# Kernel optimization log

Measured on AMD Instinct MI355X. Metric: run time of the kernel, lower is better.

The kernel has to match this reference:

```python
import jax, jax.numpy as jnp
import numpy as np

T = 100      # time steps
IC = 21      # input channels
NS = 7       # strikes
CF = 64      # cnn filters
H = 128      # lstm hidden
EPS = 1e-5


def conv1d(x, w, b):
    # x: (N, C, W), w: (O, I, 3), 'same' padding
    y = jax.lax.conv_general_dilated(x, w, window_strides=(1,), padding=[(1, 1)],
                                     dimension_numbers=('NCH', 'OIH', 'NCH'))
    return y + b[None, :, None]


def bn_eval(x, g, b, m, v):
    # eval-mode batchnorm over channel dim of (N, C, W)
    inv = g / jnp.sqrt(v + EPS)
    return x * inv[None, :, None] + (b - m * inv)[None, :, None]


def lstm_dir(xs, wih, whh, bih, bhh, reverse):
    # xs: (T, B, F); PyTorch gate order i, f, g, o
    B = xs.shape[1]
    h0 = jnp.zeros((B, H), xs.dtype)

    def step(carry, xt):
        h, c = carry
        gates = xt @ wih.T + h @ whh.T + (bih + bhh)
        i, f, g, o = jnp.split(gates, 4, axis=-1)
        c = jax.nn.sigmoid(f) * c + jax.nn.sigmoid(i) * jnp.tanh(g)
        h = jax.nn.sigmoid(o) * jnp.tanh(c)
        return (h, c), h

    _, hs = jax.lax.scan(step, (h0, h0), xs, reverse=reverse)
    return hs  # (T, B, H), aligned to input time order


def setup_inputs() -> dict:
    key = jax.random.key(0)
    ks = iter(jax.random.split(key, 64))

    def n(shape, s=0.05):
        return jax.random.normal(next(ks), shape, dtype=jnp.float32) * s

    d = {}
    d['x'] = jax.random.normal(next(ks), (512, T, IC, NS), dtype=jnp.float32)
    d['c1w'] = n((CF, IC, 3)); d['c1b'] = n((CF,))
    d['g1'] = 1.0 + n((CF,)); d['b1'] = n((CF,))
    d['m1'] = n((CF,)); d['v1'] = 1.0 + 0.1 * jax.random.uniform(next(ks), (CF,), dtype=jnp.float32)
    d['c2w'] = n((CF, CF, 3)); d['c2b'] = n((CF,))
    d['g2'] = 1.0 + n((CF,)); d['b2'] = n((CF,))
    d['m2'] = n((CF,)); d['v2'] = 1.0 + 0.1 * jax.random.uniform(next(ks), (CF,), dtype=jnp.float32)
    for layer, in_dim in ((0, CF * NS), (1, 2 * H)):
        for tag in ('f', 'b'):
            d[f'wih{layer}{tag}'] = n((4 * H, in_dim))
            d[f'whh{layer}{tag}'] = n((4 * H, H))
            d[f'bih{layer}{tag}'] = n((4 * H,))
            d[f'bhh{layer}{tag}'] = n((4 * H,))
    d['fc1w'] = n((64, 2 * H)); d['fc1b'] = n((64,))
    d['fc2w'] = n((2, 64)); d['fc2b'] = n((2,))
    return d


def reference(x, c1w, c1b, g1, b1, m1, v1, c2w, c2b, g2, b2, m2, v2,
              wih0f, whh0f, bih0f, bhh0f, wih0b, whh0b, bih0b, bhh0b,
              wih1f, whh1f, bih1f, bhh1f, wih1b, whh1b, bih1b, bhh1b,
              fc1w, fc1b, fc2w, fc2b):
    B = x.shape[0]
    # time-batched CNN: (B,T,IC,NS) -> (B*T, IC, NS); kernel (1,3) on H=1 slab == 1D conv
    h = x.reshape(B * T, IC, NS)
    h = jax.nn.relu(bn_eval(conv1d(h, c1w, c1b), g1, b1, m1, v1))
    h = jax.nn.relu(bn_eval(conv1d(h, c2w, c2b), g2, b2, m2, v2))
    # AdaptiveAvgPool2d((1, NS)) on (B,CF,1,NS) is identity; flatten -> (T,B,CF*NS)
    seq = h.reshape(B, T, CF * NS).transpose(1, 0, 2)
    # layer 0 bidirectional LSTM
    seq = jnp.concatenate([lstm_dir(seq, wih0f, whh0f, bih0f, bhh0f, False),
                           lstm_dir(seq, wih0b, whh0b, bih0b, bhh0b, True)], axis=-1)
    # layer 1 bidirectional LSTM (inter-layer dropout disabled: eval mode)
    seq = jnp.concatenate([lstm_dir(seq, wih1f, whh1f, bih1f, bhh1f, False),
                           lstm_dir(seq, wih1b, whh1b, bih1b, bhh1b, True)], axis=-1)
    last = seq[-1]                                    # (B, 2H)
    out = jax.nn.relu(last @ fc1w.T + fc1b)           # dropout = identity (eval)
    return out @ fc2w.T + fc2b                        # (B, 2)
```

## Files before the change

### kernel.cpp

```cpp
#include <hip/hip_runtime.h>

#define T_STEPS 100
#define IC      21
#define NS      7
#define CF      64
#define HID     128
#define EPS     1e-5f

#define OFF_W0FH   0
#define OFF_W0FL   114688
#define OFF_W0BH   229376
#define OFF_W0BL   344064
#define OFF_W1FH   458752
#define OFF_W1FL   524288
#define OFF_W1BH   589824
#define OFF_W1BL   655360
#define OFF_W1T    720896
#define OFF_W2T    724928
#define OFF_SCALE1 737216
#define OFF_SHIFT1 737280
#define OFF_SCALE2 737344
#define OFF_SHIFT2 737408
#define OFF_BIASL0 737472
#define OFF_BIAS1F 738496
#define OFF_BIAS1B 739008
#define PARAM_END  739520
#define OFF_H1F    739520
#define OFF_XP1B   805056
#define OFF_STATE  1067200
#define ZERO_TOTAL 393216
#define OFF_SEQ1BH 1460416
#define OFF_SEQ1BL 4737216
#define OFF_DYN    8014016

#define NB_PREP    1441792
#define NF_PREP    411840

typedef __attribute__((ext_vector_type(8))) short short8;
typedef __attribute__((ext_vector_type(4))) float f32x4;

__device__ __forceinline__ float sigmoidf_(float x) { return 1.0f / (1.0f + __expf(-x)); }
__device__ __forceinline__ float tanhf_(float x)    { return 2.0f / (1.0f + __expf(-2.0f * x)) - 1.0f; }

__device__ __forceinline__ unsigned short f2bf_rn(float f) {
    union { float f; unsigned int u; } v; v.f = f;
    unsigned int u = v.u;
    return (unsigned short)((u + 0x7FFFu + ((u >> 16) & 1u)) >> 16);
}
__device__ __forceinline__ float bf2f(unsigned short h) {
    union { unsigned int u; float f; } v; v.u = ((unsigned int)h) << 16;
    return v.f;
}

__device__ __forceinline__ void gload16(const void* g, void* l) {
    __builtin_amdgcn_global_load_lds(
        (const __attribute__((address_space(1))) unsigned int*)g,
        (__attribute__((address_space(3))) unsigned int*)l, 16, 0, 0);
}

__global__ void prep_kernel(
    const float* __restrict__ c1w, const float* __restrict__ c1b,
    const float* __restrict__ g1, const float* __restrict__ b1,
    const float* __restrict__ m1, const float* __restrict__ v1,
    const float* __restrict__ c2w, const float* __restrict__ c2b,
    const float* __restrict__ g2, const float* __restrict__ b2,
    const float* __restrict__ m2, const float* __restrict__ v2,
    const float* __restrict__ wih0f, const float* __restrict__ wih0b,
    const float* __restrict__ wih1f, const float* __restrict__ wih1b,
    const float* __restrict__ bih0f, const float* __restrict__ bhh0f,
    const float* __restrict__ bih0b, const float* __restrict__ bhh0b,
    const float* __restrict__ bih1f, const float* __restrict__ bhh1f,
    const float* __restrict__ bih1b, const float* __restrict__ bhh1b,
    float* __restrict__ ws)
{
    unsigned short* wsH = (unsigned short*)ws;
    int stride = gridDim.x * blockDim.x;
    for (int i = blockIdx.x * blockDim.x + threadIdx.x;
         i < NB_PREP + NF_PREP; i += stride) {
        if (i < NB_PREP) {
            float val; size_t dst; bool lo;
            if (i < 917504) {
                int plane = i / 229376;
                int ii = i - plane * 229376;
                int n = ii / 448, kk = ii - n * 448;
                int p = kk >> 6, oc = kk & 63;
                const float* src = (plane < 2) ? wih0f : wih0b;
                val = src[n * 448 + oc * 7 + p];
                int base = (plane == 0) ? OFF_W0FH : (plane == 1) ? OFF_W0FL
                         : (plane == 2) ? OFF_W0BH : OFF_W0BL;
                dst = (size_t)base * 2 + ii;
                lo = (plane & 1);
            } else {
                int e = i - 917504;
                int plane = e / 131072;
                int ii = e - plane * 131072;
                const float* src = (plane < 2) ? wih1f : wih1b;
                val = src[ii];
                int base = (plane == 0) ? OFF_W1FH : (plane == 1) ? OFF_W1FL
                         : (plane == 2) ? OFF_W1BH : OFF_W1BL;
                dst = (size_t)base * 2 + ii;
                lo = (plane & 1);
            }
            unsigned short hi = f2bf_rn(val);
            wsH[dst] = lo ? f2bf_rn(val - bf2f(hi)) : hi;
        } else {
            int j = i - NB_PREP;
            if (j < 4032) {
                int oc = j & 63, w = j >> 6;
                ws[OFF_W1T + j] = c1w[oc * 63 + w];
            } else if (j < 16320) {
                int jj = j - 4032;
                int oc = jj & 63, w = jj >> 6;
                ws[OFF_W2T + jj] = c2w[oc * 192 + w];
            } else if (j < 16384) {
                int oc = j - 16320;
                ws[OFF_SCALE1 + oc] = g1[oc] * rsqrtf(v1[oc] + EPS);
            } else if (j < 16448) {
                int oc = j - 16384;
                float inv = g1[oc] * rsqrtf(v1[oc] + EPS);
                ws[OFF_SHIFT1 + oc] = c1b[oc] * inv + b1[oc] - m1[oc] * inv;
            } else if (j < 16512) {
                int oc = j - 16448;
                ws[OFF_SCALE2 + oc] = g2[oc] * rsqrtf(v2[oc] + EPS);
            } else if (j < 16576) {
                int oc = j - 16512;
                float inv = g2[oc] * rsqrtf(v2[oc] + EPS);
                ws[OFF_SHIFT2 + oc] = c2b[oc] * inv + b2[oc] - m2[oc] * inv;
            } else if (j < 17600) {
                int n = j - 16576;
                ws[OFF_BIASL0 + n] = (n < 512) ? (bih0f[n] + bhh0f[n])
                                               : (bih0b[n - 512] + bhh0b[n - 512]);
            } else if (j < 18112) {
                int n = j - 17600;
                ws[OFF_BIAS1F + n] = bih1f[n] + bhh1f[n];
            } else if (j < 18624) {
                int n = j - 18112;
                ws[OFF_BIAS1B + n] = bih1b[n] + bhh1b[n];
            } else {
                ws[OFF_STATE + (j - 18624)] = 0.f;
            }
        }
    }
}

__global__ __launch_bounds__(256) void cnn_kernel(
    const float* __restrict__ x, const float* __restrict__ ws,
    unsigned short* __restrict__ outH, unsigned short* __restrict__ outL, int t0)
{
    __shared__ __align__(16) float xs[16][IC][12];
    __shared__ __align__(16) float y1[16][9][64];

    int tid = threadIdx.x;
    int oc = tid & 63, sq = tid >> 6;
    int rbase = blockIdx.x * 16;
    int tt = rbase >> 9;
    int b0 = rbase & 511;
    int t = t0 + tt;

    for (int i = tid; i < 16 * IC * 12; i += 256) ((float*)xs)[i] = 0.f;
    __syncthreads();
    for (int idx = tid; idx < 16 * 147; idx += 256) {
        int s = idx / 147, e = idx - s * 147;
        int ic = e / 7, px = e - ic * 7;
        xs[s][ic][px + 1] = x[((size_t)(b0 + s) * T_STEPS + t) * 147 + e];
    }
    __syncthreads();

    const float* w1t = ws + OFF_W1T;
    float acc1[4][7];
#pragma unroll
    for (int si = 0; si < 4; si++)
#pragma unroll
        for (int p = 0; p < 7; p++) acc1[si][p] = 0.f;

    for (int ic = 0; ic < IC; ic++) {
        float w0 = w1t[(ic * 3 + 0) * 64 + oc];
        float w1 = w1t[(ic * 3 + 1) * 64 + oc];
        float w2 = w1t[(ic * 3 + 2) * 64 + oc];
#pragma unroll
        for (int si = 0; si < 4; si++) {
            int s = 4 * sq + si;
            const float* xr = &xs[s][ic][0];
            float4 xa = *(const float4*)xr;
            float4 xb = *(const float4*)(xr + 4);
            float x8 = xr[8];
            float xv[9] = {xa.x, xa.y, xa.z, xa.w, xb.x, xb.y, xb.z, xb.w, x8};
#pragma unroll
            for (int p = 0; p < 7; p++)
                acc1[si][p] += w0 * xv[p] + w1 * xv[p + 1] + w2 * xv[p + 2];
        }
    }
    for (int i = tid; i < 2048; i += 256) {
        int s = i >> 7, row = ((i >> 6) & 1) ? 8 : 0, o2 = i & 63;
        y1[s][row][o2] = 0.f;
    }
    {
        float sc = ws[OFF_SCALE1 + oc], sh = ws[OFF_SHIFT1 + oc];
#pragma unroll
        for (int si = 0; si < 4; si++) {
            int s = 4 * sq + si;
#pragma unroll
            for (int p = 0; p < 7; p++) {
                float v = acc1[si][p] * sc + sh;
                y1[s][p + 1][oc] = v > 0.f ? v : 0.f;
            }
        }
    }
    __syncthreads();

    const float* w2t = ws + OFF_W2T;
    float acc2[4][7];
#pragma unroll
    for (int si = 0; si < 4; si++)
#pragma unroll
        for (int p = 0; p < 7; p++) acc2[si][p] = 0.f;

    for (int c4 = 0; c4 < 16; c4++) {
        float wv[12];
#pragma unroll
        for (int cc = 0; cc < 4; cc++)
#pragma unroll
            for (int k = 0; k < 3; k++)
                wv[cc * 3 + k] = w2t[((c4 * 4 + cc) * 3 + k) * 64 + oc];
#pragma unroll
        for (int si = 0; si < 4; si++) {
            int s = 4 * sq + si;
            float4 yv[9];
#pragma unroll
            for (int r = 0; r < 9; r++) yv[r] = *(const float4*)&y1[s][r][c4 * 4];
#pragma unroll
            for (int p = 0; p < 7; p++) {
                float a = 0.f;
#pragma unroll
                for (int k = 0; k < 3; k++) {
                    float4 yy = yv[p + k];
                    a += wv[0 * 3 + k] * yy.x + wv[1 * 3 + k] * yy.y
                       + wv[2 * 3 + k] * yy.z + wv[3 * 3 + k] * yy.w;
                }
                acc2[si][p] += a;
            }
        }
    }
    {
        float sc = ws[OFF_SCALE2 + oc], sh = ws[OFF_SHIFT2 + oc];
#pragma unroll
        for (int si = 0; si < 4; si++) {
            int s = 4 * sq + si;
#pragma unroll
            for (int p = 0; p < 7; p++) {
                float v = acc2[si][p] * sc + sh;
                v = v > 0.f ? v : 0.f;
                unsigned short hi = f2bf_rn(v);
                unsigned short lo = f2bf_rn(v - bf2f(hi));
                size_t o = (size_t)(rbase + s) * 448 + p * 64 + oc;
                outH[o] = hi; outL[o] = lo;
            }
        }
    }
}

__global__ __launch_bounds__(256, 2) void mgemm(
    const unsigned short* __restrict__ A0h, const unsigned short* __restrict__ A0l,
    int lda0, int K0,
    const unsigned short* __restrict__ A1h, const unsigned short* __restrict__ A1l,
    int lda1,
    const unsigned short* __restrict__ Bh, const unsigned short* __restrict__ Bl,
    const float* __restrict__ bias, float* __restrict__ out, int K)
{
    __shared__ __align__(16) unsigned short lAh[128 * 32];
    __shared__ __align__(16) unsigned short lAl[128 * 32];
    __shared__ __align__(16) unsigned short lBh[128 * 32];
    __shared__ __align__(16) unsigned short lBl[128 * 32];

    int tid = threadIdx.x;
    int m0 = blockIdx.x * 128, n0 = blockIdx.y * 128;
    int l = tid & 63, w = tid >> 6;
    int wm = w >> 1, wn = w & 1;
    int lr = l & 15, lk = l >> 4;

    int srow = w * 16 + (l >> 2);
    int skoff = (l & 3) * 8;

    f32x4 acc[4][4];
#pragma unroll
    for (int i = 0; i < 4; i++)
#pragma unroll
        for (int j = 0; j < 4; j++) acc[i][j] = (f32x4){0.f, 0.f, 0.f, 0.f};

    for (int kt = 0; kt < K; kt += 32) {
        const unsigned short *ah, *al; int lda, kl;
        if (kt < K0) { ah = A0h; al = A0l; lda = lda0; kl = kt; }
        else         { ah = A1h; al = A1l; lda = lda1; kl = kt - K0; }
        __syncthreads();
#pragma unroll
        for (int hh = 0; hh < 2; hh++) {
            size_t arow = (size_t)(m0 + hh * 64 + srow);
            size_t brow = (size_t)(n0 + hh * 64 + srow);
            char* dA = (char*)lAh + hh * 4096 + w * 1024;
            char* dAl = (char*)lAl + hh * 4096 + w * 1024;
            char* dB = (char*)lBh + hh * 4096 + w * 1024;
            char* dBl = (char*)lBl + hh * 4096 + w * 1024;
            gload16(ah + arow * lda + kl + skoff, dA);
            gload16(al + arow * lda + kl + skoff, dAl);
            gload16(Bh + brow * K + kt + skoff, dB);
            gload16(Bl + brow * K + kt + skoff, dBl);
        }
        __syncthreads();

        short8 fah[4], fal[4], fbh[4], fbl[4];
#pragma unroll
        for (int mf = 0; mf < 4; mf++) {
            int row = wm * 64 + mf * 16 + lr;
            fah[mf] = *(const short8*)&lAh[row * 32 + lk * 8];
            fal[mf] = *(const short8*)&lAl[row * 32 + lk * 8];
        }
#pragma unroll
        for (int nf = 0; nf < 4; nf++) {
            int row = wn * 64 + nf * 16 + lr;
            fbh[nf] = *(const short8*)&lBh[row * 32 + lk * 8];
            fbl[nf] = *(const short8*)&lBl[row * 32 + lk * 8];
        }
#pragma unroll
        for (int mf = 0; mf < 4; mf++)
#pragma unroll
            for (int nf = 0; nf < 4; nf++) {
                acc[mf][nf] = __builtin_amdgcn_mfma_f32_16x16x32_bf16(
                    fah[mf], fbh[nf], acc[mf][nf], 0, 0, 0);
                acc[mf][nf] = __builtin_amdgcn_mfma_f32_16x16x32_bf16(
                    fah[mf], fbl[nf], acc[mf][nf], 0, 0, 0);
                acc[mf][nf] = __builtin_amdgcn_mfma_f32_16x16x32_bf16(
                    fal[mf], fbh[nf], acc[mf][nf], 0, 0, 0);
            }
    }

#pragma unroll
    for (int nf = 0; nf < 4; nf++) {
        int gcol = n0 + wn * 64 + nf * 16 + lr;
        float bv = bias[gcol];
#pragma unroll
        for (int mf = 0; mf < 4; mf++) {
            int grow = m0 + wm * 64 + mf * 16 + lk * 4;
#pragma unroll
            for (int q = 0; q < 4; q++)
                out[(size_t)(grow + q) * 512 + gcol] = acc[mf][nf][q] + bv;
        }
    }
}

template <int OUTMODE, int REV>
__global__ __launch_bounds__(512) void lstm_scan(
    const float* __restrict__ Xpre, const float* __restrict__ whh,
    float* __restrict__ state_h, float* __restrict__ state_c,
    unsigned short* __restrict__ outH, unsigned short* __restrict__ outL,
    float* __restrict__ outF, int t0, int TC)
{
    int r0 = blockIdx.x * 2;
    int g = threadIdx.x;

    __shared__ __align__(16) float h_lds[2][128];
    __shared__ float c_lds[2][128];
    __shared__ float g_lds[2][512];

    float w[128];
#pragma unroll
    for (int k = 0; k < 128; k += 4) {
        float4 wv = *(const float4*)&whh[(size_t)g * 128 + k];
        w[k] = wv.x; w[k + 1] = wv.y; w[k + 2] = wv.z; w[k + 3] = wv.w;
    }
    if (g < 256) {
        int r = g >> 7, j = g & 127;
        h_lds[r][j] = state_h[(size_t)(r0 + r) * 128 + j];
        c_lds[r][j] = state_c[(size_t)(r0 + r) * 128 + j];
    }
    __syncthreads();

    for (int s = 0; s < TC; s++) {
        int tt = REV ? (TC - 1 - s) : s;
        float acc0 = Xpre[((size_t)tt * 512 + r0 + 0) * 512 + g];
        float acc1 = Xpre[((size_t)tt * 512 + r0 + 1) * 512 + g];
#pragma unroll
        for (int k = 0; k < 128; k += 4) {
            float4 h0 = *(const float4*)&h_lds[0][k];
            float4 h1 = *(const float4*)&h_lds[1][k];
            acc0 += w[k] * h0.x + w[k + 1] * h0.y + w[k + 2] * h0.z + w[k + 3] * h0.w;
            acc1 += w[k] * h1.x + w[k + 1] * h1.y + w[k + 2] * h1.z + w[k + 3] * h1.w;
        }
        g_lds[0][g] = acc0;
        g_lds[1][g] = acc1;
        __syncthreads();
        if (g < 256) {
            int r = g >> 7, j = g & 127;
            float gi = sigmoidf_(g_lds[r][j]);
            float gf = sigmoidf_(g_lds[r][128 + j]);
            float gg = tanhf_(g_lds[r][256 + j]);
            float go = sigmoidf_(g_lds[r][384 + j]);
            float c = gf * c_lds[r][j] + gi * gg;
            c_lds[r][j] = c;
            float h = go * tanhf_(c);
            h_lds[r][j] = h;
            if (OUTMODE == 0 || OUTMODE == 1) {
                size_t idx = (OUTMODE == 0)
                    ? ((size_t)tt * 512 + r0 + r) * 128 + j
                    : ((size_t)(t0 + tt) * 512 + r0 + r) * 128 + j;
                unsigned short hi = f2bf_rn(h);
                outH[idx] = hi;
                outL[idx] = f2bf_rn(h - bf2f(hi));
            } else if (t0 + tt == T_STEPS - 1) {
                outF[(size_t)(r0 + r) * 128 + j] = h;
            }
        }
        __syncthreads();
    }

    if (g < 256) {
        int r = g >> 7, j = g & 127;
        state_h[(size_t)(r0 + r) * 128 + j] = h_lds[r][j];
        state_c[(size_t)(r0 + r) * 128 + j] = c_lds[r][j];
    }
}

__global__ __launch_bounds__(128) void final_kernel(
    const float* __restrict__ h1f, const float* __restrict__ xp1b,
    const float* __restrict__ fc1w, const float* __restrict__ fc1b,
    const float* __restrict__ fc2w, const float* __restrict__ fc2b,
    float* __restrict__ out)
{
    int b = blockIdx.x, tid = threadIdx.x;
    __shared__ float last[256];
    __shared__ float f1[64];
    {
        int j = tid;
        float gi = sigmoidf_(xp1b[(size_t)b * 512 + j]);
        float gg = tanhf_(xp1b[(size_t)b * 512 + 256 + j]);
        float go = sigmoidf_(xp1b[(size_t)b * 512 + 384 + j]);
        float c = gi * gg;
        last[128 + j] = go * tanhf_(c);
        last[j] = h1f[(size_t)b * 128 + j];
    }
    __syncthreads();
    if (tid < 64) {
        float a = fc1b[tid];
        for (int k = 0; k < 256; k++) a += last[k] * fc1w[tid * 256 + k];
        f1[tid] = a > 0.f ? a : 0.f;
    }
    __syncthreads();
    if (tid < 2) {
        float a = fc2b[tid];
        for (int k = 0; k < 64; k++) a += f1[k] * fc2w[tid * 64 + k];
        out[b * 2 + tid] = a;
    }
}

extern "C" void kernel_launch(void* const* d_in, const int* in_sizes, int n_in,
                              void* d_out, int out_size, void* d_ws, size_t ws_size,
                              hipStream_t stream)
{
    const float* x     = (const float*)d_in[0];
    const float* c1w   = (const float*)d_in[1];
    const float* c1b   = (const float*)d_in[2];
    const float* g1    = (const float*)d_in[3];
    const float* b1    = (const float*)d_in[4];
    const float* m1    = (const float*)d_in[5];
    const float* v1    = (const float*)d_in[6];
    const float* c2w   = (const float*)d_in[7];
    const float* c2b   = (const float*)d_in[8];
    const float* g2    = (const float*)d_in[9];
    const float* b2    = (const float*)d_in[10];
    const float* m2    = (const float*)d_in[11];
    const float* v2    = (const float*)d_in[12];
    const float* wih0f = (const float*)d_in[13];
    const float* whh0f = (const float*)d_in[14];
    const float* bih0f = (const float*)d_in[15];
    const float* bhh0f = (const float*)d_in[16];
    const float* wih0b = (const float*)d_in[17];
    const float* whh0b = (const float*)d_in[18];
    const float* bih0b = (const float*)d_in[19];
    const float* bhh0b = (const float*)d_in[20];
    const float* wih1f = (const float*)d_in[21];
    const float* whh1f = (const float*)d_in[22];
    const float* bih1f = (const float*)d_in[23];
    const float* bhh1f = (const float*)d_in[24];
    const float* wih1b = (const float*)d_in[25];
    const float* bih1b = (const float*)d_in[27];
    const float* bhh1b = (const float*)d_in[28];
    const float* fc1w  = (const float*)d_in[29];
    const float* fc1b  = (const float*)d_in[30];
    const float* fc2w  = (const float*)d_in[31];
    const float* fc2b  = (const float*)d_in[32];

    float* ws  = (float*)d_ws;
    unsigned short* wsH = (unsigned short*)d_ws;
    float* out = (float*)d_out;

    const int cands[9] = {100, 50, 25, 20, 10, 5, 4, 2, 1};
    int TC = 1;
    size_t avail = ws_size / 4;
    for (int i = 0; i < 9; i++) {
        size_t need = (size_t)OFF_DYN + (size_t)cands[i] * 557056u;
        if (need <= avail) { TC = cands[i]; break; }
    }
    int NCH = T_STEPS / TC;

    unsigned short* cnnH = wsH + (size_t)OFF_DYN * 2;
    unsigned short* cnnL = cnnH + (size_t)TC * 229376;
    float* xprebuf = ws + OFF_DYN + (size_t)TC * 229376;
    unsigned short* seqfH = (unsigned short*)(xprebuf + (size_t)TC * 262144);
    unsigned short* seqfL = seqfH + (size_t)TC * 65536;
    unsigned short* seq1bH = wsH + (size_t)OFF_SEQ1BH * 2;
    unsigned short* seq1bL = wsH + (size_t)OFF_SEQ1BL * 2;

    const unsigned short* W0FH = wsH + (size_t)OFF_W0FH * 2;
    const unsigned short* W0FL = wsH + (size_t)OFF_W0FL * 2;
    const unsigned short* W0BH = wsH + (size_t)OFF_W0BH * 2;
    const unsigned short* W0BL = wsH + (size_t)OFF_W0BL * 2;
    const unsigned short* W1FH = wsH + (size_t)OFF_W1FH * 2;
    const unsigned short* W1FL = wsH + (size_t)OFF_W1FL * 2;
    const unsigned short* W1BH = wsH + (size_t)OFF_W1BH * 2;
    const unsigned short* W1BL = wsH + (size_t)OFF_W1BL * 2;

    hipLaunchKernelGGL(prep_kernel, dim3(7241), dim3(256), 0, stream,
                       c1w, c1b, g1, b1, m1, v1, c2w, c2b, g2, b2, m2, v2,
                       wih0f, wih0b, wih1f, wih1b,
                       bih0f, bhh0f, bih0b, bhh0b, bih1f, bhh1f, bih1b, bhh1b, ws);

    for (int ci = NCH - 1; ci >= 0; ci--) {
        int t0 = ci * TC;
        hipLaunchKernelGGL(cnn_kernel, dim3(TC * 32), dim3(256), 0, stream,
                           x, ws, cnnH, cnnL, t0);
        hipLaunchKernelGGL(mgemm, dim3(TC * 4, 4), dim3(256), 0, stream,
                           cnnH, cnnL, 448, 448, cnnH, cnnL, 448,
                           W0BH, W0BL, ws + OFF_BIASL0 + 512, xprebuf, 448);
        hipLaunchKernelGGL((lstm_scan<1, 1>), dim3(256), dim3(512), 0, stream,
                           xprebuf, whh0b,
                           ws + OFF_STATE, ws + OFF_STATE + 65536,
                           seq1bH, seq1bL, (float*)nullptr, t0, TC);
    }

    for (int ci = 0; ci < NCH; ci++) {
        int t0 = ci * TC;
        hipLaunchKernelGGL(cnn_kernel, dim3(TC * 32), dim3(256), 0, stream,
                           x, ws, cnnH, cnnL, t0);
        hipLaunchKernelGGL(mgemm, dim3(TC * 4, 4), dim3(256), 0, stream,
                           cnnH, cnnL, 448, 448, cnnH, cnnL, 448,
                           W0FH, W0FL, ws + OFF_BIASL0, xprebuf, 448);
        hipLaunchKernelGGL((lstm_scan<0, 0>), dim3(256), dim3(512), 0, stream,
                           xprebuf, whh0f,
                           ws + OFF_STATE + 131072, ws + OFF_STATE + 196608,
                           seqfH, seqfL, (float*)nullptr, t0, TC);
        hipLaunchKernelGGL(mgemm, dim3(TC * 4, 4), dim3(256), 0, stream,
                           seqfH, seqfL, 128, 128,
                           seq1bH + (size_t)t0 * 65536, seq1bL + (size_t)t0 * 65536, 128,
                           W1FH, W1FL, ws + OFF_BIAS1F, xprebuf, 256);
        hipLaunchKernelGGL((lstm_scan<2, 0>), dim3(256), dim3(512), 0, stream,
                           xprebuf, whh1f,
                           ws + OFF_STATE + 262144, ws + OFF_STATE + 327680,
                           (unsigned short*)nullptr, (unsigned short*)nullptr,
                           ws + OFF_H1F, t0, TC);
    }

    hipLaunchKernelGGL(mgemm, dim3(4, 4), dim3(256), 0, stream,
                       seqfH + (size_t)(TC - 1) * 65536, seqfL + (size_t)(TC - 1) * 65536,
                       128, 128,
                       seq1bH + (size_t)99 * 65536, seq1bL + (size_t)99 * 65536, 128,
                       W1BH, W1BL, ws + OFF_BIAS1B, ws + OFF_XP1B, 256);

    hipLaunchKernelGGL(final_kernel, dim3(512), dim3(128), 0, stream,
                       ws + OFF_H1F, ws + OFF_XP1B, fc1w, fc1b, fc2w, fc2b, out);

    (void)in_sizes; (void)n_in; (void)out_size; (void)ws_size;
}
```

Measured before the change: 1.368 ms.

## Overlap layer-0 and layer-1 forward LSTM chunks and use fp16 for backward sequence

Software-pipelines the forward pass so each chunk's layer-0 scan and the previous chunk's layer-1 scan run in one launch via a second grid dimension, with the two input GEMMs also batched into one launch. The backward layer-0 output is stored as a single fp16 plane, and the matching half of the layer-1 input weights uses a single f16 MFMA instead of the three-pass bf16 split. Other changes: the scan prefetches the next step's precomputed gates, the CNN uses 512 threads per block, and the chunk-size candidates are capped at 10. This trades launch count and serialisation for more workspace per chunk and lower precision on part of the layer-1 input.

```diff
diff --git a/kernel.cpp b/kernel.cpp
--- a/kernel.cpp
+++ b/kernel.cpp
@@ -11,10 +11,10 @@
 #define OFF_W0FL   114688
 #define OFF_W0BH   229376
 #define OFF_W0BL   344064
-#define OFF_W1FH   458752
-#define OFF_W1FL   524288
-#define OFF_W1BH   589824
-#define OFF_W1BL   655360
+#define OFF_W1FBH  458752
+#define OFF_W1FBL  524288
+#define OFF_W1BBH  589824
+#define OFF_W1BBL  655360
 #define OFF_W1T    720896
 #define OFF_W2T    724928
 #define OFF_SCALE1 737216
@@ -28,15 +28,14 @@
 #define OFF_H1F    739520
 #define OFF_XP1B   805056
 #define OFF_STATE  1067200
-#define ZERO_TOTAL 393216
-#define OFF_SEQ1BH 1460416
-#define OFF_SEQ1BL 4737216
-#define OFF_DYN    8014016
+#define OFF_SEQ1B  1460416
+#define OFF_DYN    4737216
 
 #define NB_PREP    1441792
 #define NF_PREP    411840
 
 typedef __attribute__((ext_vector_type(8))) short short8;
+typedef __attribute__((ext_vector_type(8))) _Float16 half8;
 typedef __attribute__((ext_vector_type(4))) float f32x4;
 
 __device__ __forceinline__ float sigmoidf_(float x) { return 1.0f / (1.0f + __expf(-x)); }
@@ -50,6 +49,9 @@
 __device__ __forceinline__ float bf2f(unsigned short h) {
     union { unsigned int u; float f; } v; v.u = ((unsigned int)h) << 16;
     return v.f;
+}
+__device__ __forceinline__ unsigned short f2h_u(float f) {
+    union { _Float16 h; unsigned short u; } v; v.h = (_Float16)f; return v.u;
 }
 
 __device__ __forceinline__ void gload16(const void* g, void* l) {
@@ -77,32 +79,34 @@
     int stride = gridDim.x * blockDim.x;
     for (int i = blockIdx.x * blockDim.x + threadIdx.x;
          i < NB_PREP + NF_PREP; i += stride) {
-        if (i < NB_PREP) {
-            float val; size_t dst; bool lo;
-            if (i < 917504) {
-                int plane = i / 229376;
-                int ii = i - plane * 229376;
-                int n = ii / 448, kk = ii - n * 448;
-                int p = kk >> 6, oc = kk & 63;
-                const float* src = (plane < 2) ? wih0f : wih0b;
-                val = src[n * 448 + oc * 7 + p];
-                int base = (plane == 0) ? OFF_W0FH : (plane == 1) ? OFF_W0FL
-                         : (plane == 2) ? OFF_W0BH : OFF_W0BL;
-                dst = (size_t)base * 2 + ii;
-                lo = (plane & 1);
+        if (i < 917504) {
+            int plane = i / 229376;
+            int ii = i - plane * 229376;
+            int n = ii / 448, kk = ii - n * 448;
+            int p = kk >> 6, oc = kk & 63;
+            const float* src = (plane < 2) ? wih0f : wih0b;
+            float val = src[n * 448 + oc * 7 + p];
+            int base = (plane == 0) ? OFF_W0FH : (plane == 1) ? OFF_W0FL
+                     : (plane == 2) ? OFF_W0BH : OFF_W0BL;
+            unsigned short hi = f2bf_rn(val);
+            wsH[(size_t)base * 2 + ii] = (plane & 1) ? f2bf_rn(val - bf2f(hi)) : hi;
+        } else if (i < NB_PREP) {
+            int e = i - 917504;
+            int plane = e / 131072;
+            int ii = e - plane * 131072;
+            int n = ii >> 8, k = ii & 255;
+            const float* src = (plane < 2) ? wih1f : wih1b;
+            float val = src[n * 256 + k];
+            int base = (plane == 0) ? OFF_W1FBH : (plane == 1) ? OFF_W1FBL
+                     : (plane == 2) ? OFF_W1BBH : OFF_W1BBL;
+            unsigned short outv;
+            if (k < 128) {
+                unsigned short hi = f2bf_rn(val);
+                outv = (plane & 1) ? f2bf_rn(val - bf2f(hi)) : hi;
             } else {
-                int e = i - 917504;
-                int plane = e / 131072;
-                int ii = e - plane * 131072;
-                const float* src = (plane < 2) ? wih1f : wih1b;
-                val = src[ii];
-                int base = (plane == 0) ? OFF_W1FH : (plane == 1) ? OFF_W1FL
-                         : (plane == 2) ? OFF_W1BH : OFF_W1BL;
-                dst = (size_t)base * 2 + ii;
-                lo = (plane & 1);
-            }
-            unsigned short hi = f2bf_rn(val);
-            wsH[dst] = lo ? f2bf_rn(val - bf2f(hi)) : hi;
+                outv = (plane & 1) ? (unsigned short)0 : f2h_u(val);
+            }
+            wsH[(size_t)base * 2 + ii] = outv;
         } else {
             int j = i - NB_PREP;
             if (j < 4032) {
@@ -143,7 +147,7 @@
     }
 }
 
-__global__ __launch_bounds__(256) void cnn_kernel(
+__global__ __launch_bounds__(512) void cnn_kernel(
     const float* __restrict__ x, const float* __restrict__ ws,
     unsigned short* __restrict__ outH, unsigned short* __restrict__ outL, int t0)
 {
@@ -157,9 +161,9 @@
     int b0 = rbase & 511;
     int t = t0 + tt;
 
-    for (int i = tid; i < 16 * IC * 12; i += 256) ((float*)xs)[i] = 0.f;
+    for (int i = tid; i < 16 * IC * 12; i += 512) ((float*)xs)[i] = 0.f;
     __syncthreads();
-    for (int idx = tid; idx < 16 * 147; idx += 256) {
+    for (int idx = tid; idx < 16 * 147; idx += 512) {
         int s = idx / 147, e = idx - s * 147;
         int ic = e / 7, px = e - ic * 7;
         xs[s][ic][px + 1] = x[((size_t)(b0 + s) * T_STEPS + t) * 147 + e];
@@ -167,9 +171,9 @@
     __syncthreads();
 
     const float* w1t = ws + OFF_W1T;
-    float acc1[4][7];
-#pragma unroll
-    for (int si = 0; si < 4; si++)
+    float acc1[2][7];
+#pragma unroll
+    for (int si = 0; si < 2; si++)
 #pragma unroll
         for (int p = 0; p < 7; p++) acc1[si][p] = 0.f;
 
@@ -178,8 +182,8 @@
         float w1 = w1t[(ic * 3 + 1) * 64 + oc];
         float w2 = w1t[(ic * 3 + 2) * 64 + oc];
 #pragma unroll
-        for (int si = 0; si < 4; si++) {
-            int s = 4 * sq + si;
+        for (int si = 0; si < 2; si++) {
+            int s = 2 * sq + si;
             const float* xr = &xs[s][ic][0];
             float4 xa = *(const float4*)xr;
             float4 xb = *(const float4*)(xr + 4);
@@ -190,15 +194,15 @@
                 acc1[si][p] += w0 * xv[p] + w1 * xv[p + 1] + w2 * xv[p + 2];
         }
     }
-    for (int i = tid; i < 2048; i += 256) {
+    for (int i = tid; i < 2048; i += 512) {
         int s = i >> 7, row = ((i >> 6) & 1) ? 8 : 0, o2 = i & 63;
         y1[s][row][o2] = 0.f;
     }
     {
         float sc = ws[OFF_SCALE1 + oc], sh = ws[OFF_SHIFT1 + oc];
 #pragma unroll
-        for (int si = 0; si < 4; si++) {
-            int s = 4 * sq + si;
+        for (int si = 0; si < 2; si++) {
+            int s = 2 * sq + si;
 #pragma unroll
             for (int p = 0; p < 7; p++) {
                 float v = acc1[si][p] * sc + sh;
@@ -209,9 +213,9 @@
     __syncthreads();
 
     const float* w2t = ws + OFF_W2T;
-    float acc2[4][7];
-#pragma unroll
-    for (int si = 0; si < 4; si++)
+    float acc2[2][7];
+#pragma unroll
+    for (int si = 0; si < 2; si++)
 #pragma unroll
         for (int p = 0; p < 7; p++) acc2[si][p] = 0.f;
 
@@ -223,8 +227,8 @@
             for (int k = 0; k < 3; k++)
                 wv[cc * 3 + k] = w2t[((c4 * 4 + cc) * 3 + k) * 64 + oc];
 #pragma unroll
-        for (int si = 0; si < 4; si++) {
-            int s = 4 * sq + si;
+        for (int si = 0; si < 2; si++) {
+            int s = 2 * sq + si;
             float4 yv[9];
 #pragma unroll
             for (int r = 0; r < 9; r++) yv[r] = *(const float4*)&y1[s][r][c4 * 4];
@@ -244,8 +248,8 @@
     {
         float sc = ws[OFF_SCALE2 + oc], sh = ws[OFF_SHIFT2 + oc];
 #pragma unroll
-        for (int si = 0; si < 4; si++) {
-            int s = 4 * sq + si;
+        for (int si = 0; si < 2; si++) {
+            int s = 2 * sq + si;
 #pragma unroll
             for (int p = 0; p < 7; p++) {
                 float v = acc2[si][p] * sc + sh;
@@ -259,14 +263,19 @@
     }
 }
 
-__global__ __launch_bounds__(256, 2) void mgemm(
-    const unsigned short* __restrict__ A0h, const unsigned short* __restrict__ A0l,
-    int lda0, int K0,
-    const unsigned short* __restrict__ A1h, const unsigned short* __restrict__ A1l,
-    int lda1,
-    const unsigned short* __restrict__ Bh, const unsigned short* __restrict__ Bl,
-    const float* __restrict__ bias, float* __restrict__ out, int K)
+struct GArg {
+    const unsigned short *A0h, *A0l;
+    const _Float16* A1;
+    const unsigned short *Bh, *Bl;
+    const float* bias;
+    float* out;
+    int lda0, lda1, K0, K;
+};
+
+__global__ __launch_bounds__(256, 2) void mgemm2(GArg ga, GArg gb)
 {
+    GArg g = (blockIdx.z == 0) ? ga : gb;
+
     __shared__ __align__(16) unsigned short lAh[128 * 32];
     __shared__ __align__(16) unsigned short lAl[128 * 32];
     __shared__ __align__(16) unsigned short lBh[128 * 32];
@@ -278,7 +287,7 @@
     int wm = w >> 1, wn = w & 1;
     int lr = l & 15, lk = l >> 4;
 
-    int srow = w * 16 + (l >> 2);
+    int srow = (l >> 2);
     int skoff = (l & 3) * 8;
 
     f32x4 acc[4][4];
@@ -287,73 +296,103 @@
 #pragma unroll
         for (int j = 0; j < 4; j++) acc[i][j] = (f32x4){0.f, 0.f, 0.f, 0.f};
 
-    for (int kt = 0; kt < K; kt += 32) {
-        const unsigned short *ah, *al; int lda, kl;
-        if (kt < K0) { ah = A0h; al = A0l; lda = lda0; kl = kt; }
-        else         { ah = A1h; al = A1l; lda = lda1; kl = kt - K0; }
+    for (int kt = 0; kt < g.K; kt += 32) {
+        bool seg0 = (kt < g.K0);
         __syncthreads();
 #pragma unroll
         for (int hh = 0; hh < 2; hh++) {
-            size_t arow = (size_t)(m0 + hh * 64 + srow);
-            size_t brow = (size_t)(n0 + hh * 64 + srow);
-            char* dA = (char*)lAh + hh * 4096 + w * 1024;
+            int row = hh * 64 + w * 16 + srow;
+            char* dA  = (char*)lAh + hh * 4096 + w * 1024;
             char* dAl = (char*)lAl + hh * 4096 + w * 1024;
-            char* dB = (char*)lBh + hh * 4096 + w * 1024;
+            char* dB  = (char*)lBh + hh * 4096 + w * 1024;
             char* dBl = (char*)lBl + hh * 4096 + w * 1024;
-            gload16(ah + arow * lda + kl + skoff, dA);
-            gload16(al + arow * lda + kl + skoff, dAl);
-            gload16(Bh + brow * K + kt + skoff, dB);
-            gload16(Bl + brow * K + kt + skoff, dBl);
+            size_t arow = (size_t)(m0 + row);
+            size_t brow = (size_t)(n0 + row);
+            if (seg0) {
+                gload16(g.A0h + arow * g.lda0 + kt + skoff, dA);
+                gload16(g.A0l + arow * g.lda0 + kt + skoff, dAl);
+                gload16(g.Bl + brow * g.K + kt + skoff, dBl);
+            } else {
+                gload16(g.A1 + arow * g.lda1 + (kt - g.K0) + skoff, dA);
+            }
+            gload16(g.Bh + brow * g.K + kt + skoff, dB);
         }
         __syncthreads();
 
-        short8 fah[4], fal[4], fbh[4], fbl[4];
-#pragma unroll
-        for (int mf = 0; mf < 4; mf++) {
-            int row = wm * 64 + mf * 16 + lr;
-            fah[mf] = *(const short8*)&lAh[row * 32 + lk * 8];
-            fal[mf] = *(const short8*)&lAl[row * 32 + lk * 8];
-        }
-#pragma unroll
-        for (int nf = 0; nf < 4; nf++) {
-            int row = wn * 64 + nf * 16 + lr;
-            fbh[nf] = *(const short8*)&lBh[row * 32 + lk * 8];
-            fbl[nf] = *(const short8*)&lBl[row * 32 + lk * 8];
-        }
-#pragma unroll
-        for (int mf = 0; mf < 4; mf++)
+        if (seg0) {
+            short8 fah[4], fal[4], fbh[4], fbl[4];
+#pragma unroll
+            for (int mf = 0; mf < 4; mf++) {
+                int row = wm * 64 + mf * 16 + lr;
+                fah[mf] = *(const short8*)&lAh[row * 32 + lk * 8];
+                fal[mf] = *(const short8*)&lAl[row * 32 + lk * 8];
+            }
 #pragma unroll
             for (int nf = 0; nf < 4; nf++) {
-                acc[mf][nf] = __builtin_amdgcn_mfma_f32_16x16x32_bf16(
-                    fah[mf], fbh[nf], acc[mf][nf], 0, 0, 0);
-                acc[mf][nf] = __builtin_amdgcn_mfma_f32_16x16x32_bf16(
-                    fah[mf], fbl[nf], acc[mf][nf], 0, 0, 0);
-                acc[mf][nf] = __builtin_amdgcn_mfma_f32_16x16x32_bf16(
-                    fal[mf], fbh[nf], acc[mf][nf], 0, 0, 0);
-            }
+                int row = wn * 64 + nf * 16 + lr;
+                fbh[nf] = *(const short8*)&lBh[row * 32 + lk * 8];
+                fbl[nf] = *(const short8*)&lBl[row * 32 + lk * 8];
+            }
+#pragma unroll
+            for (int mf = 0; mf < 4; mf++)
+#pragma unroll
+                for (int nf = 0; nf < 4; nf++) {
+                    acc[mf][nf] = __builtin_amdgcn_mfma_f32_16x16x32_bf16(
+                        fah[mf], fbh[nf], acc[mf][nf], 0, 0, 0);
+                    acc[mf][nf] = __builtin_amdgcn_mfma_f32_16x16x32_bf16(
+                        fah[mf], fbl[nf], acc[mf][nf], 0, 0, 0);
+                    acc[mf][nf] = __builtin_amdgcn_mfma_f32_16x16x32_bf16(
+                        fal[mf], fbh[nf], acc[mf][nf], 0, 0, 0);
+                }
+        } else {
+            half8 fah[4], fbh[4];
+#pragma unroll
+            for (int mf = 0; mf < 4; mf++) {
+                int row = wm * 64 + mf * 16 + lr;
+                fah[mf] = *(const half8*)&lAh[row * 32 + lk * 8];
+            }
+#pragma unroll
+            for (int nf = 0; nf < 4; nf++) {
+                int row = wn * 64 + nf * 16 + lr;
+                fbh[nf] = *(const half8*)&lBh[row * 32 + lk * 8];
+            }
+#pragma unroll
+            for (int mf = 0; mf < 4; mf++)
+#pragma unroll
+                for (int nf = 0; nf < 4; nf++)
+                    acc[mf][nf] = __builtin_amdgcn_mfma_f32_16x16x32_f16(
+                        fah[mf], fbh[nf], acc[mf][nf], 0, 0, 0);
+        }
     }
 
 #pragma unroll
     for (int nf = 0; nf < 4; nf++) {
         int gcol = n0 + wn * 64 + nf * 16 + lr;
-        float bv = bias[gcol];
+        float bv = g.bias[gcol];
 #pragma unroll
         for (int mf = 0; mf < 4; mf++) {
             int grow = m0 + wm * 64 + mf * 16 + lk * 4;
 #pragma unroll
             for (int q = 0; q < 4; q++)
-                out[(size_t)(grow + q) * 512 + gcol] = acc[mf][nf][q] + bv;
-        }
-    }
-}
-
-template <int OUTMODE, int REV>
-__global__ __launch_bounds__(512) void lstm_scan(
-    const float* __restrict__ Xpre, const float* __restrict__ whh,
-    float* __restrict__ state_h, float* __restrict__ state_c,
-    unsigned short* __restrict__ outH, unsigned short* __restrict__ outL,
-    float* __restrict__ outF, int t0, int TC)
+                g.out[(size_t)(grow + q) * 512 + gcol] = acc[mf][nf][q] + bv;
+        }
+    }
+}
+
+struct SArg {
+    const float* Xpre;
+    const float* whh;
+    float *sh, *sc;
+    unsigned short *oH, *oL;
+    _Float16* o16;
+    float* oF;
+    int mode, t0;
+};
+
+template <int REV>
+__global__ __launch_bounds__(512) void lstm_scan(SArg a, SArg b, int TC)
 {
+    SArg sa = (blockIdx.y == 0) ? a : b;
     int r0 = blockIdx.x * 2;
     int g = threadIdx.x;
 
@@ -364,20 +403,29 @@
     float w[128];
 #pragma unroll
     for (int k = 0; k < 128; k += 4) {
-        float4 wv = *(const float4*)&whh[(size_t)g * 128 + k];
+        float4 wv = *(const float4*)&sa.whh[(size_t)g * 128 + k];
         w[k] = wv.x; w[k + 1] = wv.y; w[k + 2] = wv.z; w[k + 3] = wv.w;
     }
     if (g < 256) {
         int r = g >> 7, j = g & 127;
-        h_lds[r][j] = state_h[(size_t)(r0 + r) * 128 + j];
-        c_lds[r][j] = state_c[(size_t)(r0 + r) * 128 + j];
+        h_lds[r][j] = sa.sh[(size_t)(r0 + r) * 128 + j];
+        c_lds[r][j] = sa.sc[(size_t)(r0 + r) * 128 + j];
     }
     __syncthreads();
+
+    int tt0 = REV ? (TC - 1) : 0;
+    float p0 = sa.Xpre[((size_t)tt0 * 512 + r0 + 0) * 512 + g];
+    float p1 = sa.Xpre[((size_t)tt0 * 512 + r0 + 1) * 512 + g];
 
     for (int s = 0; s < TC; s++) {
         int tt = REV ? (TC - 1 - s) : s;
-        float acc0 = Xpre[((size_t)tt * 512 + r0 + 0) * 512 + g];
-        float acc1 = Xpre[((size_t)tt * 512 + r0 + 1) * 512 + g];
+        float n0 = 0.f, n1 = 0.f;
+        if (s + 1 < TC) {
+            int ttn = REV ? (tt - 1) : (tt + 1);
+            n0 = sa.Xpre[((size_t)ttn * 512 + r0 + 0) * 512 + g];
+            n1 = sa.Xpre[((size_t)ttn * 512 + r0 + 1) * 512 + g];
+        }
+        float acc0 = p0, acc1 = p1;
 #pragma unroll
         for (int k = 0; k < 128; k += 4) {
             float4 h0 = *(const float4*)&h_lds[0][k];
@@ -398,24 +446,26 @@
             c_lds[r][j] = c;
             float h = go * tanhf_(c);
             h_lds[r][j] = h;
-            if (OUTMODE == 0 || OUTMODE == 1) {
-                size_t idx = (OUTMODE == 0)
-                    ? ((size_t)tt * 512 + r0 + r) * 128 + j
-                    : ((size_t)(t0 + tt) * 512 + r0 + r) * 128 + j;
+            if (sa.mode == 0) {
+                size_t idx = ((size_t)tt * 512 + r0 + r) * 128 + j;
                 unsigned short hi = f2bf_rn(h);
-                outH[idx] = hi;
-                outL[idx] = f2bf_rn(h - bf2f(hi));
-            } else if (t0 + tt == T_STEPS - 1) {
-                outF[(size_t)(r0 + r) * 128 + j] = h;
+                sa.oH[idx] = hi;
+                sa.oL[idx] = f2bf_rn(h - bf2f(hi));
+            } else if (sa.mode == 1) {
+                size_t idx = ((size_t)(sa.t0 + tt) * 512 + r0 + r) * 128 + j;
+                sa.o16[idx] = (_Float16)h;
+            } else if (sa.t0 + tt == T_STEPS - 1) {
+                sa.oF[(size_t)(r0 + r) * 128 + j] = h;
             }
         }
         __syncthreads();
+        p0 = n0; p1 = n1;
     }
 
     if (g < 256) {
         int r = g >> 7, j = g & 127;
-        state_h[(size_t)(r0 + r) * 128 + j] = h_lds[r][j];
-        state_c[(size_t)(r0 + r) * 128 + j] = c_lds[r][j];
+        sa.sh[(size_t)(r0 + r) * 128 + j] = h_lds[r][j];
+        sa.sc[(size_t)(r0 + r) * 128 + j] = c_lds[r][j];
     }
 }
 
@@ -492,77 +542,98 @@
     unsigned short* wsH = (unsigned short*)d_ws;
     float* out = (float*)d_out;
 
-    const int cands[9] = {100, 50, 25, 20, 10, 5, 4, 2, 1};
+    const int cands[5] = {10, 5, 4, 2, 1};
     int TC = 1;
     size_t avail = ws_size / 4;
-    for (int i = 0; i < 9; i++) {
-        size_t need = (size_t)OFF_DYN + (size_t)cands[i] * 557056u;
+    for (int i = 0; i < 5; i++) {
+        size_t need = (size_t)OFF_DYN + (size_t)cands[i] * 819200u;
         if (need <= avail) { TC = cands[i]; break; }
     }
     int NCH = T_STEPS / TC;
 
-    unsigned short* cnnH = wsH + (size_t)OFF_DYN * 2;
-    unsigned short* cnnL = cnnH + (size_t)TC * 229376;
-    float* xprebuf = ws + OFF_DYN + (size_t)TC * 229376;
-    unsigned short* seqfH = (unsigned short*)(xprebuf + (size_t)TC * 262144);
+    unsigned short* cnnH  = wsH + (size_t)OFF_DYN * 2;
+    unsigned short* cnnL  = cnnH + (size_t)TC * 229376;
+    float* xpre0 = ws + OFF_DYN + (size_t)TC * 229376;
+    float* xpre1 = xpre0 + (size_t)TC * 262144;
+    unsigned short* seqfH = (unsigned short*)(xpre1 + (size_t)TC * 262144);
     unsigned short* seqfL = seqfH + (size_t)TC * 65536;
-    unsigned short* seq1bH = wsH + (size_t)OFF_SEQ1BH * 2;
-    unsigned short* seq1bL = wsH + (size_t)OFF_SEQ1BL * 2;
+    _Float16* seq1b = (_Float16*)(ws + OFF_SEQ1B);
 
     const unsigned short* W0FH = wsH + (size_t)OFF_W0FH * 2;
     const unsigned short* W0FL = wsH + (size_t)OFF_W0FL * 2;
     const unsigned short* W0BH = wsH + (size_t)OFF_W0BH * 2;
     const unsigned short* W0BL = wsH + (size_t)OFF_W0BL * 2;
-    const unsigned short* W1FH = wsH + (size_t)OFF_W1FH * 2;
-    const unsigned short* W1FL = wsH + (size_t)OFF_W1FL * 2;
-    const unsigned short* W1BH = wsH + (size_t)OFF_W1BH * 2;
-    const unsigned short* W1BL = wsH + (size_t)OFF_W1BL * 2;
+    const unsigned short* W1FBH = wsH + (size_t)OFF_W1FBH * 2;
+    const unsigned short* W1FBL = wsH + (size_t)OFF_W1FBL * 2;
+    const unsigned short* W1BBH = wsH + (size_t)OFF_W1BBH * 2;
+    const unsigned short* W1BBL = wsH + (size_t)OFF_W1BBL * 2;
+
+    float* st = ws + OFF_STATE;
 
     hipLaunchKernelGGL(prep_kernel, dim3(7241), dim3(256), 0, stream,
                        c1w, c1b, g1, b1, m1, v1, c2w, c2b, g2, b2, m2, v2,
                        wih0f, wih0b, wih1f, wih1b,
                        bih0f, bhh0f, bih0b, bhh0b, bih1f, bhh1f, bih1b, bhh1b, ws);
 
-    for (int ci = NCH - 1; ci >= 0; ci--) {
-        int t0 = ci * TC;
-        hipLaunchKernelGGL(cnn_kernel, dim3(TC * 32), dim3(256), 0, stream,
+    for (int j = 0; j < NCH; j++) {
+        int c = NCH - 1 - j;
+        int t0 = c * TC;
+        hipLaunchKernelGGL(cnn_kernel, dim3(TC * 32), dim3(512), 0, stream,
                            x, ws, cnnH, cnnL, t0);
-        hipLaunchKernelGGL(mgemm, dim3(TC * 4, 4), dim3(256), 0, stream,
-                           cnnH, cnnL, 448, 448, cnnH, cnnL, 448,
-                           W0BH, W0BL, ws + OFF_BIASL0 + 512, xprebuf, 448);
-        hipLaunchKernelGGL((lstm_scan<1, 1>), dim3(256), dim3(512), 0, stream,
-                           xprebuf, whh0b,
-                           ws + OFF_STATE, ws + OFF_STATE + 65536,
-                           seq1bH, seq1bL, (float*)nullptr, t0, TC);
-    }
-
-    for (int ci = 0; ci < NCH; ci++) {
-        int t0 = ci * TC;
-        hipLaunchKernelGGL(cnn_kernel, dim3(TC * 32), dim3(256), 0, stream,
+        GArg gb = { cnnH, cnnL, (const _Float16*)cnnH, W0BH, W0BL,
+                    ws + OFF_BIASL0 + 512, xpre0, 448, 0, 448, 448 };
+        hipLaunchKernelGGL(mgemm2, dim3(TC * 4, 4, 1), dim3(256), 0, stream, gb, gb);
+        SArg sb = { xpre0, whh0b, st, st + 65536,
+                    nullptr, nullptr, seq1b, nullptr, 1, t0 };
+        hipLaunchKernelGGL((lstm_scan<1>), dim3(256, 1), dim3(512), 0, stream,
+                           sb, sb, TC);
+    }
+
+    for (int i = 0; i < NCH; i++) {
+        int t0 = i * TC;
+        hipLaunchKernelGGL(cnn_kernel, dim3(TC * 32), dim3(512), 0, stream,
                            x, ws, cnnH, cnnL, t0);
-        hipLaunchKernelGGL(mgemm, dim3(TC * 4, 4), dim3(256), 0, stream,
-                           cnnH, cnnL, 448, 448, cnnH, cnnL, 448,
-                           W0FH, W0FL, ws + OFF_BIASL0, xprebuf, 448);
-        hipLaunchKernelGGL((lstm_scan<0, 0>), dim3(256), dim3(512), 0, stream,
-                           xprebuf, whh0f,
-                           ws + OFF_STATE + 131072, ws + OFF_STATE + 196608,
-                           seqfH, seqfL, (float*)nullptr, t0, TC);
-        hipLaunchKernelGGL(mgemm, dim3(TC * 4, 4), dim3(256), 0, stream,
-                           seqfH, seqfL, 128, 128,
-                           seq1bH + (size_t)t0 * 65536, seq1bL + (size_t)t0 * 65536, 128,
-                           W1FH, W1FL, ws + OFF_BIAS1F, xprebuf, 256);
-        hipLaunchKernelGGL((lstm_scan<2, 0>), dim3(256), dim3(512), 0, stream,
-                           xprebuf, whh1f,
-                           ws + OFF_STATE + 262144, ws + OFF_STATE + 327680,
-                           (unsigned short*)nullptr, (unsigned short*)nullptr,
-                           ws + OFF_H1F, t0, TC);
-    }
-
-    hipLaunchKernelGGL(mgemm, dim3(4, 4), dim3(256), 0, stream,
-                       seqfH + (size_t)(TC - 1) * 65536, seqfL + (size_t)(TC - 1) * 65536,
-                       128, 128,
-                       seq1bH + (size_t)99 * 65536, seq1bL + (size_t)99 * 65536, 128,
-                       W1BH, W1BL, ws + OFF_BIAS1B, ws + OFF_XP1B, 256);
+        GArg g0 = { cnnH, cnnL, (const _Float16*)cnnH, W0FH, W0FL,
+                    ws + OFF_BIASL0, xpre0, 448, 0, 448, 448 };
+        if (i > 0) {
+            int t0p = (i - 1) * TC;
+            GArg g1a = { seqfH, seqfL, seq1b + (size_t)t0p * 65536,
+                         W1FBH, W1FBL, ws + OFF_BIAS1F, xpre1, 128, 128, 128, 256 };
+            hipLaunchKernelGGL(mgemm2, dim3(TC * 4, 4, 2), dim3(256), 0, stream,
+                               g0, g1a);
+            SArg s0 = { xpre0, whh0f, st + 131072, st + 196608,
+                        seqfH, seqfL, nullptr, nullptr, 0, t0 };
+            SArg s1 = { xpre1, whh1f, st + 262144, st + 327680,
+                        nullptr, nullptr, nullptr, ws + OFF_H1F, 2, t0p };
+            hipLaunchKernelGGL((lstm_scan<0>), dim3(256, 2), dim3(512), 0, stream,
+                               s0, s1, TC);
+        } else {
+            hipLaunchKernelGGL(mgemm2, dim3(TC * 4, 4, 1), dim3(256), 0, stream,
+                               g0, g0);
+            SArg s0 = { xpre0, whh0f, st + 131072, st + 196608,
+                        seqfH, seqfL, nullptr, nullptr, 0, t0 };
+            hipLaunchKernelGGL((lstm_scan<0>), dim3(256, 1), dim3(512), 0, stream,
+                               s0, s0, TC);
+        }
+    }
+    {
+        int t0p = (NCH - 1) * TC;
+        GArg g1a = { seqfH, seqfL, seq1b + (size_t)t0p * 65536,
+                     W1FBH, W1FBL, ws + OFF_BIAS1F, xpre1, 128, 128, 128, 256 };
+        hipLaunchKernelGGL(mgemm2, dim3(TC * 4, 4, 1), dim3(256), 0, stream,
+                           g1a, g1a);
+        SArg s1 = { xpre1, whh1f, st + 262144, st + 327680,
+                    nullptr, nullptr, nullptr, ws + OFF_H1F, 2, t0p };
+        hipLaunchKernelGGL((lstm_scan<0>), dim3(256, 1), dim3(512), 0, stream,
+                           s1, s1, TC);
+    }
+
+    {
+        GArg gf = { seqfH + (size_t)(TC - 1) * 65536, seqfL + (size_t)(TC - 1) * 65536,
+                    seq1b + (size_t)99 * 65536,
+                    W1BBH, W1BBL, ws + OFF_BIAS1B, ws + OFF_XP1B, 128, 128, 128, 256 };
+        hipLaunchKernelGGL(mgemm2, dim3(4, 4, 1), dim3(256), 0, stream, gf, gf);
+    }
 
     hipLaunchKernelGGL(final_kernel, dim3(512), dim3(128), 0, stream,
                        ws + OFF_H1F, ws + OFF_XP1B, fc1w, fc1b, fc2w, fc2b, out);
```

Measured after the change: 3.681 ms. 169% more time.
